# Kernel optimization log

Measured on AMD Instinct MI355X. Metric: run time of the kernel, lower is better.

## Reference

```python
import jax, jax.numpy as jnp
import numpy as np

B, T = 16, 2048
NEG = -1e9  # finite large-negative for masked softmax (avoids NaN on empty rows)


def setup_inputs() -> dict:
    key = jax.random.key(0)
    k1, k2 = jax.random.split(key)
    logits = jax.random.normal(k1, (B, T, 1), dtype=jnp.float32)
    seq_len = jax.random.randint(k2, (B,), 1, T + 1, dtype=jnp.int32)
    return {"logits": logits, "seq_len": seq_len}


def reference(logits, seq_len):
    scores = jax.nn.sigmoid(logits.squeeze(-1))  # [B, T]
    # pairwise relevance: sigmoid((1 - |s_i - s_j| - 0.5) / 0.1)
    pairwise_diff = scores[:, :, None] - scores[:, None, :]  # [B, T, T]
    rel_mat = jax.nn.sigmoid((1.0 - jnp.abs(pairwise_diff) - 0.5) / 0.1)
    # ragged mask: valid positions are < seq_len[b]
    valid = jnp.arange(T)[None, :] < seq_len[:, None]            # [B, T]
    mask2d = valid[:, :, None] & valid[:, None, :]               # [B, T, T]
    masked = jnp.where(mask2d, rel_mat, NEG)
    sm = jax.nn.softmax(masked, axis=-1)                          # masked cols -> ~0
    # zero out invalid rows (original leaves them as zeros)
    out_mat = jnp.where(valid[:, :, None], sm, 0.0)
    return out_mat
```

## Files before the change

kernel.cpp:

```cpp
#include <hip/hip_runtime.h>

#define TT 2048
#define BLOCK 256
#define WAVES (BLOCK / 64)

__device__ __forceinline__ float fast_sigmoid(float x) {
    return __builtin_amdgcn_rcpf(1.0f + __expf(-x));
}

__global__ __launch_bounds__(BLOCK) void score_branch_kernel(
    const float* __restrict__ logits, const int* __restrict__ seq_len,
    float* __restrict__ out)
{
    __shared__ float s_scores[TT];

    const int b    = blockIdx.y;
    const int row0 = blockIdx.x * WAVES;
    const int tid  = threadIdx.x;
    const int lane = tid & 63;
    const int wv   = tid >> 6;
    const int L    = seq_len[b];

    const float4* lg4 = (const float4*)(logits + (size_t)b * TT);
    float4* s4 = (float4*)s_scores;
    #pragma unroll
    for (int k = 0; k < TT / (BLOCK * 4); ++k) {
        int idx4 = tid + k * BLOCK;
        float4 v = lg4[idx4];
        float4 s;
        s.x = fast_sigmoid(v.x);
        s.y = fast_sigmoid(v.y);
        s.z = fast_sigmoid(v.z);
        s.w = fast_sigmoid(v.w);
        s4[idx4] = s;
    }
    __syncthreads();

    const int i = row0 + wv;
    float4* orow4 = (float4*)(out + ((size_t)b * TT + (size_t)i) * TT);

    if (i >= L) {
        float4 z = make_float4(0.f, 0.f, 0.f, 0.f);
        #pragma unroll
        for (int q = 0; q < 8; ++q)
            orow4[q * 64 + lane] = z;
        return;
    }

    const float si = s_scores[i];

    float4 e4[8];
    float partial = 0.f;
    #pragma unroll
    for (int q = 0; q < 8; ++q) {
        const int idx4 = q * 64 + lane;
        float4 sj = s4[idx4];
        const int j0 = idx4 * 4;
        float vals[4] = {sj.x, sj.y, sj.z, sj.w};
        float* ev = (float*)&e4[q];
        #pragma unroll
        for (int qq = 0; qq < 4; ++qq) {
            float d  = si - vals[qq];
            float t  = fmaf(fabsf(d), -10.0f, 5.0f);
            float p  = fast_sigmoid(t);
            float ee = __expf(p);
            ee = (j0 + qq < L) ? ee : 0.0f;
            ev[qq] = ee;
            partial += ee;
        }
    }

    #pragma unroll
    for (int off = 32; off > 0; off >>= 1)
        partial += __shfl_xor(partial, off, 64);
    const float inv = __builtin_amdgcn_rcpf(partial);

    #pragma unroll
    for (int q = 0; q < 8; ++q) {
        float4 o;
        o.x = e4[q].x * inv;
        o.y = e4[q].y * inv;
        o.z = e4[q].z * inv;
        o.w = e4[q].w * inv;
        orow4[q * 64 + lane] = o;
    }
}

extern "C" void kernel_launch(void* const* d_in, const int* in_sizes, int n_in,
                              void* d_out, int out_size, void* d_ws, size_t ws_size,
                              hipStream_t stream) {
    const float* logits  = (const float*)d_in[0];
    const int*   seq_len = (const int*)d_in[1];
    float*       out     = (float*)d_out;

    const int B = in_sizes[1];
    dim3 grid(TT / WAVES, B);
    score_branch_kernel<<<grid, dim3(BLOCK), 0, stream>>>(logits, seq_len, out);
}
```

Measured before the change: 257.7 us.

## Skip masked work, use exp2 math and nontemporal stores

Blocks whose rows all lie past seq_len now write zeros before loading scores. Column groups fully beyond L skip the sigmoid/exp work and are zero-filled directly, and full groups skip the per-element mask select. Exponentials are rewritten as exp2 with pre-scaled constants, and all output writes use nontemporal stores so the write-heavy output bypasses cache retention. The kernel is bound by writing the B*T*T output, so the compute savings may matter less than the store path.

```diff
diff --git a/kernel.cpp b/kernel.cpp
--- a/kernel.cpp
+++ b/kernel.cpp
@@ -4,8 +4,17 @@
 #define BLOCK 256
 #define WAVES (BLOCK / 64)
 
-__device__ __forceinline__ float fast_sigmoid(float x) {
-    return __builtin_amdgcn_rcpf(1.0f + __expf(-x));
+#define LOG2E 1.4426950408889634f
+
+typedef float vf4 __attribute__((ext_vector_type(4)));
+
+__device__ __forceinline__ void nt_store4(float4* p, float x, float y, float z, float w) {
+    vf4 v = {x, y, z, w};
+    __builtin_nontemporal_store(v, (vf4*)p);
+}
+
+__device__ __forceinline__ float fast_sigmoid_e2(float u) {
+    return __builtin_amdgcn_rcpf(1.0f + __builtin_amdgcn_exp2f(u));
 }
 
 __global__ __launch_bounds__(BLOCK) void score_branch_kernel(
@@ -21,30 +30,44 @@
     const int wv   = tid >> 6;
     const int L    = seq_len[b];
 
+    const int i = row0 + wv;
+    float4* orow4 = (float4*)(out + ((size_t)b * TT + (size_t)i) * TT);
+
+    if (row0 >= L) {
+        #pragma unroll
+        for (int q = 0; q < 8; ++q)
+            nt_store4(&orow4[q * 64 + lane], 0.f, 0.f, 0.f, 0.f);
+        return;
+    }
+
     const float4* lg4 = (const float4*)(logits + (size_t)b * TT);
     float4* s4 = (float4*)s_scores;
     #pragma unroll
     for (int k = 0; k < TT / (BLOCK * 4); ++k) {
         int idx4 = tid + k * BLOCK;
-        float4 v = lg4[idx4];
-        float4 s;
-        s.x = fast_sigmoid(v.x);
-        s.y = fast_sigmoid(v.y);
-        s.z = fast_sigmoid(v.z);
-        s.w = fast_sigmoid(v.w);
-        s4[idx4] = s;
+        if (idx4 * 4 < L) {
+            float4 v = lg4[idx4];
+            float4 s;
+            s.x = fast_sigmoid_e2(-LOG2E * v.x);
+            s.y = fast_sigmoid_e2(-LOG2E * v.y);
+            s.z = fast_sigmoid_e2(-LOG2E * v.z);
+            s.w = fast_sigmoid_e2(-LOG2E * v.w);
+            s4[idx4] = s;
+        }
     }
     __syncthreads();
 
-    const int i = row0 + wv;
-    float4* orow4 = (float4*)(out + ((size_t)b * TT + (size_t)i) * TT);
-
     if (i >= L) {
-        float4 z = make_float4(0.f, 0.f, 0.f, 0.f);
         #pragma unroll
         for (int q = 0; q < 8; ++q)
-            orow4[q * 64 + lane] = z;
+            nt_store4(&orow4[q * 64 + lane], 0.f, 0.f, 0.f, 0.f);
         return;
+    }
+
+    #pragma unroll
+    for (int q = 0; q < 8; ++q) {
+        if (q * 256 >= L)
+            nt_store4(&orow4[q * 64 + lane], 0.f, 0.f, 0.f, 0.f);
     }
 
     const float si = s_scores[i];
@@ -53,20 +76,24 @@
     float partial = 0.f;
     #pragma unroll
     for (int q = 0; q < 8; ++q) {
-        const int idx4 = q * 64 + lane;
-        float4 sj = s4[idx4];
-        const int j0 = idx4 * 4;
-        float vals[4] = {sj.x, sj.y, sj.z, sj.w};
-        float* ev = (float*)&e4[q];
-        #pragma unroll
-        for (int qq = 0; qq < 4; ++qq) {
-            float d  = si - vals[qq];
-            float t  = fmaf(fabsf(d), -10.0f, 5.0f);
-            float p  = fast_sigmoid(t);
-            float ee = __expf(p);
-            ee = (j0 + qq < L) ? ee : 0.0f;
-            ev[qq] = ee;
-            partial += ee;
+        if (q * 256 < L) {
+            const int idx4 = q * 64 + lane;
+            float4 sj = s4[idx4];
+            const int j0 = idx4 * 4;
+            const bool fullgrp = ((q + 1) * 256 <= L);
+            float vals[4] = {sj.x, sj.y, sj.z, sj.w};
+            float* ev = (float*)&e4[q];
+            #pragma unroll
+            for (int qq = 0; qq < 4; ++qq) {
+                float d  = si - vals[qq];
+                float u  = fmaf(fabsf(d), 10.0f * LOG2E, -5.0f * LOG2E);
+                float p  = fast_sigmoid_e2(u);
+                float ee = __builtin_amdgcn_exp2f(p * LOG2E);
+                if (!fullgrp)
+                    ee = (j0 + qq < L) ? ee : 0.0f;
+                ev[qq] = ee;
+                partial += ee;
+            }
         }
     }
 
@@ -77,12 +104,10 @@
 
     #pragma unroll
     for (int q = 0; q < 8; ++q) {
-        float4 o;
-        o.x = e4[q].x * inv;
-        o.y = e4[q].y * inv;
-        o.z = e4[q].z * inv;
-        o.w = e4[q].w * inv;
-        orow4[q * 64 + lane] = o;
+        if (q * 256 < L) {
+            nt_store4(&orow4[q * 64 + lane],
+                      e4[q].x * inv, e4[q].y * inv, e4[q].z * inv, e4[q].w * inv);
+        }
     }
 }
 
```

Measured after the change: 265.7 us. 3.1% more time.
